# Kernel tuning notes

Hardware: AMD Instinct MI355X
Metric: run time of the kernel (lower is better)

The kernel has to match this reference:

```python
import jax, jax.numpy as jnp
import numpy as np

LAYER_SIZES = [1024, 1024, 1024, 1024, 1024, 1024, 512]
MAX_PATHS = 128
BATCH = 128
N_LAYERS = len(LAYER_SIZES) - 1


def setup_inputs() -> dict:
    key = jax.random.key(0)
    keys = jax.random.split(key, 1 + 2 * N_LAYERS)
    inp = {"x": jax.random.normal(keys[0], (BATCH, LAYER_SIZES[0]), dtype=jnp.float32)}
    for i in range(N_LAYERS):
        inp[f"W{i}"] = jax.random.normal(keys[1 + 2 * i], (LAYER_SIZES[i], LAYER_SIZES[i + 1]), dtype=jnp.float32) * 0.01
        inp[f"b{i}"] = jax.random.normal(keys[2 + 2 * i], (LAYER_SIZES[i + 1],), dtype=jnp.float32) * 0.01
    return inp


def _layer(data, W, b):
    # data: [B, in_feat, P] -> [B, out_feat, 3P]
    B, _, P = data.shape
    O = W.shape[1]
    pos = jnp.einsum('bfp,fo->bpo', data, W) + b          # [B, P, O]; neg branch is exactly -pos
    branches = jnp.stack([-pos, jnp.zeros_like(pos), pos], axis=-1)  # [B, P, O, 3]
    # transpose(1,2) then reshape: interleave branches per source path, matching torch
    return branches.transpose(0, 2, 1, 3).reshape(B, O, P * 3)


def _prune(data, keep):
    # keep top-`keep` paths by L2 norm over the feature dim
    norms = jnp.linalg.norm(data, axis=1)                 # [B, P]
    _, idx = jax.lax.top_k(norms, keep)                   # [B, keep]
    return jnp.take_along_axis(data, idx[:, None, :], axis=-1)


def _forward(x, Ws, bs):
    data = x[:, :, None]                                   # [B, F, 1]
    for i in range(N_LAYERS):
        data = _layer(data, Ws[i], bs[i])
        if i < N_LAYERS - 1:
            data = jnp.tanh(data)
        if data.shape[-1] > MAX_PATHS:
            data = _prune(data, MAX_PATHS)
    # collapse with 'max_abs': per (batch, feature) pick path with largest |value|
    idx = jnp.argmax(jnp.abs(data), axis=-1, keepdims=True)
    output = jnp.take_along_axis(data, idx, axis=-1).squeeze(-1)
    return output, data


def reference(x, W0, b0, W1, b1, W2, b2, W3, b3, W4, b4, W5, b5):
    Ws = [W0, W1, W2, W3, W4, W5]
    bs = [b0, b1, b2, b3, b4, b5]
    return _forward(x, Ws, bs)
```

## Files before the change

### kernel.cpp

```cpp
#include <hip/hip_runtime.h>
#include <math.h>


using s8v = __attribute__((ext_vector_type(8))) short;
using f4v = __attribute__((ext_vector_type(4))) float;

__device__ __forceinline__ float bf2f(short b) {
  unsigned u = ((unsigned)(unsigned short)b) << 16;
  return __builtin_bit_cast(float, u);
}
__device__ __forceinline__ short f2bf(float f) {
  unsigned u = __builtin_bit_cast(unsigned, f);
  u = (u + 0x7FFFu + ((u >> 16) & 1u)) >> 16;
  return (short)u;
}
__device__ __forceinline__ void split_store(float f, short* hi, short* lo) {
  short h = f2bf(f);
  *hi = h;
  *lo = f2bf(f - bf2f(h));
}

struct TWArgs {
  const float* W[6];
  short* Th[6];
  short* Tl[6];
  const float* x;
  short* A0h;
  short* A0l;
  float* zone;
};
__global__ void __launch_bounds__(256)
transW_all(TWArgs a) {
  const int z = blockIdx.z;
  const int t = threadIdx.x;
  if (z == 6) {
    int bid = blockIdx.y * 16 + blockIdx.x;
    if (bid < 128) {
      int i = (bid * 256 + t) * 4;
      float4 v = *(const float4*)&a.x[i];
      short4 h, l;
      h.x = f2bf(v.x); l.x = f2bf(v.x - bf2f(h.x));
      h.y = f2bf(v.y); l.y = f2bf(v.y - bf2f(h.y));
      h.z = f2bf(v.z); l.z = f2bf(v.z - bf2f(h.z));
      h.w = f2bf(v.w); l.w = f2bf(v.w - bf2f(h.w));
      *(short4*)&a.A0h[i] = h;
      *(short4*)&a.A0l[i] = l;
    } else if (bid < 176) {
      a.zone[(bid - 128) * 256 + t] = 0.f;
    }
    return;
  }
  const int N = (z == 5) ? 512 : 1024;
  const int n0 = blockIdx.x * 64, k0 = blockIdx.y * 64;
  if (n0 >= N) return;
  const float* __restrict__ W = a.W[z];
  short* __restrict__ Th = a.Th[z];
  short* __restrict__ Tl = a.Tl[z];
  __shared__ float tile[64][65];
  const int r = t >> 4, c4 = (t & 15) * 4;
#pragma unroll
  for (int i = 0; i < 4; ++i) {
    int rr = r + 16 * i;
    float4 v = *(const float4*)&W[(size_t)(k0 + rr) * N + n0 + c4];
    tile[rr][c4 + 0] = v.x;
    tile[rr][c4 + 1] = v.y;
    tile[rr][c4 + 2] = v.z;
    tile[rr][c4 + 3] = v.w;
  }
  __syncthreads();
#pragma unroll
  for (int i = 0; i < 4; ++i) {
    int n = r + 16 * i;
    short4 h, l;
    float f0 = tile[c4 + 0][n], f1 = tile[c4 + 1][n];
    float f2 = tile[c4 + 2][n], f3 = tile[c4 + 3][n];
    h.x = f2bf(f0); l.x = f2bf(f0 - bf2f(h.x));
    h.y = f2bf(f1); l.y = f2bf(f1 - bf2f(h.y));
    h.z = f2bf(f2); l.z = f2bf(f2 - bf2f(h.z));
    h.w = f2bf(f3); l.w = f2bf(f3 - bf2f(h.w));
    size_t o = (size_t)(n0 + n) * 1024 + k0 + c4;
    *(short4*)&Th[o] = h;
    *(short4*)&Tl[o] = l;
  }
}

template <int EPI, int D, int KS>
__global__ void __launch_bounds__(256, 2)
mfma_gemm(const short* __restrict__ Ah, const short* __restrict__ Al,
          const short* __restrict__ Bh, const short* __restrict__ Bl,
          const float* __restrict__ bias, short* __restrict__ Oh,
          short* __restrict__ Ol, float* __restrict__ Of,
          float* __restrict__ ns, float* __restrict__ dotv,
          float* __restrict__ nrmv, int N, int Dn) {
  constexpr int KC = 1024 / KS;
  constexpr int BKP = 40;
  __shared__ short As_h[64 * BKP], As_l[64 * BKP];
  __shared__ short Bs_h[64 * BKP], Bs_l[64 * BKP];
  const int t = threadIdx.x;
  const int row0 = blockIdx.y * 64;
  const int col0 = blockIdx.x * 64;
  const int kb = blockIdx.z * KC;
  const int sr = t >> 2, sko = (t & 3) * 8;
  const short* Ahp = Ah + (size_t)(row0 + sr) * 1024 + kb + sko;
  const short* Alp = Al + (size_t)(row0 + sr) * 1024 + kb + sko;
  const short* Bhp = Bh + (size_t)(col0 + sr) * 1024 + kb + sko;
  const short* Blp = Bl + (size_t)(col0 + sr) * 1024 + kb + sko;
  const int w = t >> 6, lane = t & 63;
  const int l16 = lane & 15, q = lane >> 4;
  const int wm0 = (w & 1) * 32, wn0 = (w >> 1) * 32;
  const int abase = (wm0 + l16) * BKP + q * 8;
  const int bbase = (wn0 + l16) * BKP + q * 8;
  f4v acc[2][2];
#pragma unroll
  for (int i = 0; i < 2; ++i)
#pragma unroll
    for (int j = 0; j < 2; ++j) acc[i][j] = (f4v){0.f, 0.f, 0.f, 0.f};
  uint4 rah = *(const uint4*)(Ahp);
  uint4 ral = *(const uint4*)(Alp);
  uint4 rbh = *(const uint4*)(Bhp);
  uint4 rbl = *(const uint4*)(Blp);
  for (int k0 = 0; k0 < KC; k0 += 32) {
    __syncthreads();
    *(uint4*)&As_h[sr * BKP + sko] = rah;
    *(uint4*)&As_l[sr * BKP + sko] = ral;
    *(uint4*)&Bs_h[sr * BKP + sko] = rbh;
    *(uint4*)&Bs_l[sr * BKP + sko] = rbl;
    if (k0 + 32 < KC) {
      rah = *(const uint4*)(Ahp + k0 + 32);
      ral = *(const uint4*)(Alp + k0 + 32);
      rbh = *(const uint4*)(Bhp + k0 + 32);
      rbl = *(const uint4*)(Blp + k0 + 32);
    }
    __syncthreads();
    s8v ah[2], al[2], bh[2], bl[2];
#pragma unroll
    for (int mt = 0; mt < 2; ++mt) {
      ah[mt] = *(const s8v*)&As_h[abase + mt * 16 * BKP];
      al[mt] = *(const s8v*)&As_l[abase + mt * 16 * BKP];
    }
#pragma unroll
    for (int nt = 0; nt < 2; ++nt) {
      bh[nt] = *(const s8v*)&Bs_h[bbase + nt * 16 * BKP];
      bl[nt] = *(const s8v*)&Bs_l[bbase + nt * 16 * BKP];
    }
#pragma unroll
    for (int mt = 0; mt < 2; ++mt)
#pragma unroll
      for (int nt = 0; nt < 2; ++nt) {
        acc[mt][nt] = __builtin_amdgcn_mfma_f32_16x16x32_bf16(
            ah[mt], bh[nt], acc[mt][nt], 0, 0, 0);
        acc[mt][nt] = __builtin_amdgcn_mfma_f32_16x16x32_bf16(
            ah[mt], bl[nt], acc[mt][nt], 0, 0, 0);
        acc[mt][nt] = __builtin_amdgcn_mfma_f32_16x16x32_bf16(
            al[mt], bh[nt], acc[mt][nt], 0, 0, 0);
      }
  }

  if constexpr (EPI == 0) {
    const int R = (int)gridDim.y << 6;
#pragma unroll
    for (int nt = 0; nt < 2; ++nt) {
      int gcol = col0 + wn0 + nt * 16 + l16;
#pragma unroll
      for (int mt = 0; mt < 2; ++mt)
#pragma unroll
        for (int r = 0; r < 4; ++r) {
          int rr = row0 + wm0 + mt * 16 + q * 4 + r;
          Of[((size_t)blockIdx.z * R + rr) * N + gcol] = acc[mt][nt][r];
        }
    }
  } else if constexpr (EPI == 1) {
    float bcr[2];
    int gc[2];
#pragma unroll
    for (int nt = 0; nt < 2; ++nt) {
      gc[nt] = col0 + wn0 + nt * 16 + l16;
      bcr[nt] = bias[gc[nt]];
    }
#pragma unroll
    for (int mt = 0; mt < 2; ++mt)
#pragma unroll
      for (int r = 0; r < 4; ++r) {
        int rr = row0 + wm0 + mt * 16 + q * 4 + r;
        int b = rr / D, u = rr - b * D;
        size_t ob = (size_t)(b * Dn) * (size_t)N;
        size_t om = ob + (size_t)(1 + 2 * u) * N;
        size_t op = ob + (size_t)(2 + 2 * u) * N;
        float sm = 0.f, sp = 0.f;
#pragma unroll
        for (int nt = 0; nt < 2; ++nt) {
          float v = acc[mt][nt][r];
          float tm = tanhf(bcr[nt] - v), tp = tanhf(bcr[nt] + v);
          split_store(tm, &Oh[om + gc[nt]], &Ol[om + gc[nt]]);
          split_store(tp, &Oh[op + gc[nt]], &Ol[op + gc[nt]]);
          sm = fmaf(tm, tm, sm);
          sp = fmaf(tp, tp, sp);
        }
#pragma unroll
        for (int msk = 1; msk < 16; msk <<= 1) {
          sm += __shfl_xor(sm, msk);
          sp += __shfl_xor(sp, msk);
        }
        if (l16 == 0) {
          atomicAdd(&ns[b * Dn + 1 + 2 * u], sm);
          atomicAdd(&ns[b * Dn + 2 + 2 * u], sp);
        }
        if (u == 0) {
          float sz = 0.f;
#pragma unroll
          for (int nt = 0; nt < 2; ++nt) {
            float tz = tanhf(bcr[nt]);
            split_store(tz, &Oh[ob + gc[nt]], &Ol[ob + gc[nt]]);
            sz = fmaf(tz, tz, sz);
          }
#pragma unroll
          for (int msk = 1; msk < 16; msk <<= 1) sz += __shfl_xor(sz, msk);
          if (l16 == 0) atomicAdd(&ns[b * Dn], sz);
        }
      }
  } else {
    float b5r[2];
    int gc[2];
#pragma unroll
    for (int nt = 0; nt < 2; ++nt) {
      gc[nt] = col0 + wn0 + nt * 16 + l16;
      b5r[nt] = bias[gc[nt]];
    }
#pragma unroll
    for (int mt = 0; mt < 2; ++mt)
#pragma unroll
      for (int r = 0; r < 4; ++r) {
        int rr = row0 + wm0 + mt * 16 + q * 4 + r;
        float nr = 0.f, dt = 0.f;
#pragma unroll
        for (int nt = 0; nt < 2; ++nt) {
          float v = acc[mt][nt][r];
          Of[(size_t)rr * N + gc[nt]] = v;
          nr = fmaf(v, v, nr);
          dt = fmaf(v, b5r[nt], dt);
        }
#pragma unroll
        for (int msk = 1; msk < 16; msk <<= 1) {
          nr += __shfl_xor(nr, msk);
          dt += __shfl_xor(dt, msk);
        }
        if (l16 == 0) {
          atomicAdd(&nrmv[rr], nr);
          atomicAdd(&dotv[rr], dt);
        }
      }
  }
}

template <int KS>
__global__ void __launch_bounds__(256)
comb0_hl(const float* __restrict__ P, const float* __restrict__ bias,
         short* __restrict__ Oh, short* __restrict__ Ol, int R, int N) {
  int i = blockIdx.x * 256 + threadIdx.x;
  int n4 = N >> 2;
  int r = i / n4, c4 = (i - r * n4) * 4;
  float4 y = *(const float4*)&P[(size_t)r * N + c4];
  size_t stride = (size_t)R * N;
#pragma unroll
  for (int ks = 1; ks < KS; ++ks) {
    const float4 p = *(const float4*)&P[ks * stride + (size_t)r * N + c4];
    y.x += p.x; y.y += p.y; y.z += p.z; y.w += p.w;
  }
  float4 bc = *(const float4*)(bias + c4);
  float t0 = tanhf(bc.x + y.x), t1 = tanhf(bc.y + y.y);
  float t2 = tanhf(bc.z + y.z), t3 = tanhf(bc.w + y.w);
  short4 h, l;
  h.x = f2bf(t0); l.x = f2bf(t0 - bf2f(h.x));
  h.y = f2bf(t1); l.y = f2bf(t1 - bf2f(h.y));
  h.z = f2bf(t2); l.z = f2bf(t2 - bf2f(h.z));
  h.w = f2bf(t3); l.w = f2bf(t3 - bf2f(h.w));
  *(short4*)&Oh[(size_t)r * N + c4] = h;
  *(short4*)&Ol[(size_t)r * N + c4] = l;
}

template <int KS, int D>
__global__ void __launch_bounds__(256)
comb1_hl(const float* __restrict__ P, const float* __restrict__ bias,
         short* __restrict__ Oh, short* __restrict__ Ol, int R, int N,
         int Dn) {
  int i = blockIdx.x * 256 + threadIdx.x;
  int n4 = N >> 2;
  int r = i / n4, c4 = (i - r * n4) * 4;
  int b = r / D, u = r - b * D;
  float4 y = *(const float4*)&P[(size_t)r * N + c4];
  size_t stride = (size_t)R * N;
#pragma unroll
  for (int ks = 1; ks < KS; ++ks) {
    const float4 p = *(const float4*)&P[ks * stride + (size_t)r * N + c4];
    y.x += p.x; y.y += p.y; y.z += p.z; y.w += p.w;
  }
  float4 bc = *(const float4*)(bias + c4);
  size_t ob = (size_t)(b * Dn) * N + c4;
  size_t om = ob + (size_t)(1 + 2 * u) * N;
  size_t op = ob + (size_t)(2 + 2 * u) * N;
  {
    float t0 = tanhf(bc.x - y.x), t1 = tanhf(bc.y - y.y);
    float t2 = tanhf(bc.z - y.z), t3 = tanhf(bc.w - y.w);
    short4 h, l;
    h.x = f2bf(t0); l.x = f2bf(t0 - bf2f(h.x));
    h.y = f2bf(t1); l.y = f2bf(t1 - bf2f(h.y));
    h.z = f2bf(t2); l.z = f2bf(t2 - bf2f(h.z));
    h.w = f2bf(t3); l.w = f2bf(t3 - bf2f(h.w));
    *(short4*)&Oh[om] = h;
    *(short4*)&Ol[om] = l;
  }
  {
    float t0 = tanhf(bc.x + y.x), t1 = tanhf(bc.y + y.y);
    float t2 = tanhf(bc.z + y.z), t3 = tanhf(bc.w + y.w);
    short4 h, l;
    h.x = f2bf(t0); l.x = f2bf(t0 - bf2f(h.x));
    h.y = f2bf(t1); l.y = f2bf(t1 - bf2f(h.y));
    h.z = f2bf(t2); l.z = f2bf(t2 - bf2f(h.z));
    h.w = f2bf(t3); l.w = f2bf(t3 - bf2f(h.w));
    *(short4*)&Oh[op] = h;
    *(short4*)&Ol[op] = l;
  }
  if (u == 0) {
    float t0 = tanhf(bc.x), t1 = tanhf(bc.y);
    float t2 = tanhf(bc.z), t3 = tanhf(bc.w);
    short4 h, l;
    h.x = f2bf(t0); l.x = f2bf(t0 - bf2f(h.x));
    h.y = f2bf(t1); l.y = f2bf(t1 - bf2f(h.y));
    h.z = f2bf(t2); l.z = f2bf(t2 - bf2f(h.z));
    h.w = f2bf(t3); l.w = f2bf(t3 - bf2f(h.w));
    *(short4*)&Oh[ob] = h;
    *(short4*)&Ol[ob] = l;
  }
}

__global__ void __launch_bounds__(256)
prune4_k(const float* __restrict__ ns, int* __restrict__ kept4) {
  int b = blockIdx.x, t = threadIdx.x;
  __shared__ float nss[31];
  __shared__ float key[243];
  __shared__ int cls[243];
  if (t < 31) nss[t] = ns[b * 31 + t];
  __syncthreads();
  if (t < 243) {
    int j = t / 3, t4 = t - 3 * j;
    int d0 = j / 27, d1 = (j / 9) % 3, d2 = (j / 3) % 3, d3 = j % 3;
    int u = 0;
    u = (d0 == 1) ? 0 : (1 + 2 * u + (d0 == 2));
    u = (d1 == 1) ? 0 : (1 + 2 * u + (d1 == 2));
    u = (d2 == 1) ? 0 : (1 + 2 * u + (d2 == 2));
    u = (d3 == 1) ? 0 : (1 + 2 * u + (d3 == 2));
    cls[t] = u;
    key[t] = (t4 == 1) ? 0.f : nss[u];
  }
  __syncthreads();
  if (t < 243) {
    float k = key[t];
    int rank = 0;
    for (int e = 0; e < 243; ++e) {
      float ke = key[e];
      rank += (ke > k) || (ke == k && e < t);
    }
    if (rank < 128) {
      int t4 = t - 3 * (t / 3);
      kept4[b * 128 + rank] = (cls[t] << 1) | (t4 == 2 ? 1 : 0);
    }
  }
}

__global__ void __launch_bounds__(384)
prune5_k(const float* __restrict__ dotv, const float* __restrict__ nrmv,
         const float* __restrict__ b5, const int* __restrict__ kept4,
         int* __restrict__ kept5) {
  int b = blockIdx.x, t = threadIdx.x;
  __shared__ float red[384];
  __shared__ float pns[128];
  __shared__ float key[384];
  float p = 0.f;
  for (int o = t; o < 512; o += 384) p = fmaf(b5[o], b5[o], p);
  red[t] = p;
  __syncthreads();
  if (t < 128) red[t] = red[t] + red[t + 128] + red[t + 256];
  __syncthreads();
  if (t < 64) red[t] += red[t + 64];
  __syncthreads();
  if (t < 32) red[t] += red[t + 32];
  __syncthreads();
  if (t < 16) red[t] += red[t + 16];
  __syncthreads();
  if (t < 8) red[t] += red[t + 8];
  __syncthreads();
  if (t < 4) red[t] += red[t + 4];
  __syncthreads();
  if (t < 2) red[t] += red[t + 2];
  __syncthreads();
  if (t == 0) red[0] += red[1];
  __syncthreads();
  float nb5 = red[0];
  if (t < 128) {
    int k4 = kept4[b * 128 + t];
    int c = k4 >> 1;
    float s = (k4 & 1) ? 1.f : -1.f;
    pns[t] = nb5 + nrmv[b * 31 + c] + s * 2.f * dotv[b * 31 + c];
  }
  __syncthreads();
  int m = t / 3, tt = t - 3 * m;
  key[t] = (tt == 1) ? 0.f : pns[m];
  __syncthreads();
  float k = key[t];
  int rank = 0;
  for (int e = 0; e < 384; ++e) {
    float ke = key[e];
    rank += (ke > k) || (ke == k && e < t);
  }
  if (rank < 128) kept5[b * 128 + rank] = (m << 1) | (tt == 2 ? 1 : 0);
}

__global__ void __launch_bounds__(256)
finalize_k(const float* __restrict__ Y5, const float* __restrict__ b5,
           const int* __restrict__ kept4, const int* __restrict__ kept5,
           float* __restrict__ out, float* __restrict__ dataout) {
  const int b = blockIdx.y;
  const int o0 = blockIdx.x * 64;
  __shared__ float Ys[31][65];
  __shared__ float bias_s[64];
  __shared__ float vt[64][130];
  __shared__ float ra[64][4];
  __shared__ float rv[64][4];
  const int t = threadIdx.x;
  for (int idx = t; idx < 31 * 64; idx += 256) {
    int c = idx >> 6, o = idx & 63;
    Ys[c][o] = Y5[((size_t)b * 31 + c) * 512 + o0 + o];
  }
  if (t < 64) bias_s[t] = b5[o0 + t];
  const int rr = t & 127, oh = t >> 7;
  int k5 = kept5[b * 128 + rr];
  int m = k5 >> 1;
  float sig = (k5 & 1) ? 1.f : -1.f;
  int k4 = kept4[b * 128 + m];
  int cc = k4 >> 1;
  float s4 = (k4 & 1) ? 1.f : -1.f;
  float afac = sig * s4;
  __syncthreads();
#pragma unroll
  for (int ol = 0; ol < 32; ++ol) {
    int o = oh * 32 + ol;
    float v = sig * bias_s[o] + afac * Ys[cc][o];
    dataout[((size_t)b * 512 + o0 + o) * 128 + rr] = v;
    vt[o][rr] = v;
  }
  __syncthreads();
  int o = t >> 2, q = t & 3;
  float bestv = vt[o][q * 32];
  float besta = fabsf(bestv);
  for (int i = 1; i < 32; ++i) {
    float v = vt[o][q * 32 + i];
    float a = fabsf(v);
    if (a > besta) {
      besta = a;
      bestv = v;
    }
  }
  ra[o][q] = besta;
  rv[o][q] = bestv;
  __syncthreads();
  if (t < 64) {
    float ba = ra[t][0], bv = rv[t][0];
#pragma unroll
    for (int qq = 1; qq < 4; ++qq) {
      if (ra[t][qq] > ba) {
        ba = ra[t][qq];
        bv = rv[t][qq];
      }
    }
    out[(size_t)b * 512 + o0 + t] = bv;
  }
}

extern "C" void kernel_launch(void* const* d_in, const int* in_sizes, int n_in,
                              void* d_out, int out_size, void* d_ws,
                              size_t ws_size, hipStream_t stream) {
  const float* x = (const float*)d_in[0];
  const float* Wt[6];
  const float* bs[6];
  for (int i = 0; i < 6; ++i) {
    Wt[i] = (const float*)d_in[1 + 2 * i];
    bs[i] = (const float*)d_in[2 + 2 * i];
  }
  char* base = (char*)d_ws;
  short* A0h = (short*)(base + 0);
  short* A0l = (short*)(base + 262144);
  short* Wh[6], *Wl[6];
  {
    size_t off = 524288;
    for (int i = 0; i < 6; ++i) {
      size_t sz = (i < 5) ? 2097152 : 1048576;
      Wh[i] = (short*)(base + off);
      Wl[i] = (short*)(base + off + sz);
      off += 2 * sz;
    }
  }
  short* C1h = (short*)(base + 23592960), *C1l = (short*)(base + 23855104);
  short* C2h = (short*)(base + 24117248), *C2l = (short*)(base + 24903680);
  short* C3h = (short*)(base + 25690112), *C3l = (short*)(base + 27525120);
  short* C4h = (short*)(base + 29360128), *C4l = (short*)(base + 33292288);
  short* C5h = (short*)(base + 524288);
  short* C5l = (short*)(base + 8912896);
  float* PA = (float*)(base + 29360128);
  float* PB = (float*)(base + 524288);
  float* Y5 = (float*)(base + 23592960);
  float* ns = (float*)(base + 37224448);
  float* dotv = ns + 3968;
  float* nrmv = dotv + 3968;
  int* kept4 = (int*)(base + 37273600);
  int* kept5 = (int*)(base + 37339136);
  float* outp = (float*)d_out;
  float* dataout = outp + 128 * 512;

  dim3 blk(256);
  TWArgs twa;
  for (int i = 0; i < 6; ++i) {
    twa.W[i] = Wt[i];
    twa.Th[i] = Wh[i];
    twa.Tl[i] = Wl[i];
  }
  twa.x = x;
  twa.A0h = A0h;
  twa.A0l = A0l;
  twa.zone = ns;
  transW_all<<<dim3(16, 16, 7), blk, 0, stream>>>(twa);

  mfma_gemm<0, 1, 4><<<dim3(16, 2, 4), blk, 0, stream>>>(
      A0h, A0l, Wh[0], Wl[0], nullptr, nullptr, nullptr, PA, nullptr, nullptr,
      nullptr, 1024, 1);
  comb0_hl<4><<<dim3(128), blk, 0, stream>>>(PA, bs[0], C1h, C1l, 128, 1024);
  mfma_gemm<0, 1, 4><<<dim3(16, 2, 4), blk, 0, stream>>>(
      C1h, C1l, Wh[1], Wl[1], nullptr, nullptr, nullptr, PA, nullptr, nullptr,
      nullptr, 1024, 3);
  comb1_hl<4, 1><<<dim3(128), blk, 0, stream>>>(PA, bs[1], C2h, C2l, 128, 1024,
                                                3);
  mfma_gemm<0, 3, 4><<<dim3(16, 6, 4), blk, 0, stream>>>(
      C2h, C2l, Wh[2], Wl[2], nullptr, nullptr, nullptr, PA, nullptr, nullptr,
      nullptr, 1024, 7);
  comb1_hl<4, 3><<<dim3(384), blk, 0, stream>>>(PA, bs[2], C3h, C3l, 384, 1024,
                                                7);
  mfma_gemm<0, 7, 2><<<dim3(16, 14, 2), blk, 0, stream>>>(
      C3h, C3l, Wh[3], Wl[3], nullptr, nullptr, nullptr, PB, nullptr, nullptr,
      nullptr, 1024, 15);
  comb1_hl<2, 7><<<dim3(896), blk, 0, stream>>>(PB, bs[3], C4h, C4l, 896, 1024,
                                                15);
  mfma_gemm<1, 15, 1><<<dim3(16, 30), blk, 0, stream>>>(
      C4h, C4l, Wh[4], Wl[4], bs[4], C5h, C5l, nullptr, ns, nullptr, nullptr,
      1024, 31);
  prune4_k<<<dim3(128), blk, 0, stream>>>(ns, kept4);
  mfma_gemm<2, 31, 1><<<dim3(8, 62), blk, 0, stream>>>(
      C5h, C5l, Wh[5], Wl[5], bs[5], nullptr, nullptr, Y5, nullptr, dotv, nrmv,
      512, 0);
  prune5_k<<<dim3(128), dim3(384), 0, stream>>>(dotv, nrmv, bs[5], kept4,
                                                kept5);
  finalize_k<<<dim3(8, 128), blk, 0, stream>>>(Y5, bs[5], kept4, kept5, outp,
                                               dataout);
}
```

Measured before the change: 246.5 us.

## Stage GEMM epilogue through shared memory for vectorized stores; raise split-K

The MFMA GEMM epilogue now writes accumulators into a padded shared-memory tile and re-reads them so each thread owns 16 contiguous columns of one row. This allows 128-bit global stores of the fp32 partials and the packed bf16 hi/lo outputs, and reduces the atomic norm reductions to a 4-lane shuffle. Launch bounds are raised to 3 blocks per SM, and the first two tiny GEMMs use split-K of 8 instead of 4 to fill more CUs. The costs are an extra 17KB of LDS per block, a barrier, and more partial sums for the combine kernels to read.

Result: no change. 242.5 us (-1.6%).

```diff
diff --git a/kernel.cpp b/kernel.cpp
--- a/kernel.cpp
+++ b/kernel.cpp
@@ -13,11 +13,6 @@
   unsigned u = __builtin_bit_cast(unsigned, f);
   u = (u + 0x7FFFu + ((u >> 16) & 1u)) >> 16;
   return (short)u;
-}
-__device__ __forceinline__ void split_store(float f, short* hi, short* lo) {
-  short h = f2bf(f);
-  *hi = h;
-  *lo = f2bf(f - bf2f(h));
 }
 
 struct TWArgs {
@@ -85,7 +80,7 @@
 }
 
 template <int EPI, int D, int KS>
-__global__ void __launch_bounds__(256, 2)
+__global__ void __launch_bounds__(256, 3)
 mfma_gemm(const short* __restrict__ Ah, const short* __restrict__ Al,
           const short* __restrict__ Bh, const short* __restrict__ Bl,
           const float* __restrict__ bias, short* __restrict__ Oh,
@@ -96,6 +91,7 @@
   constexpr int BKP = 40;
   __shared__ short As_h[64 * BKP], As_l[64 * BKP];
   __shared__ short Bs_h[64 * BKP], Bs_l[64 * BKP];
+  __shared__ float et[64][68];
   const int t = threadIdx.x;
   const int row0 = blockIdx.y * 64;
   const int col0 = blockIdx.x * 64;
@@ -156,99 +152,103 @@
       }
   }
 
+#pragma unroll
+  for (int mt = 0; mt < 2; ++mt)
+#pragma unroll
+    for (int nt = 0; nt < 2; ++nt)
+#pragma unroll
+      for (int r = 0; r < 4; ++r)
+        et[wm0 + mt * 16 + q * 4 + r][wn0 + nt * 16 + l16] = acc[mt][nt][r];
+  __syncthreads();
+  const int rl = t >> 2, cc = (t & 3) * 16;
+  float v[16];
+#pragma unroll
+  for (int j = 0; j < 16; ++j) v[j] = et[rl][cc + j];
+  const int rr = row0 + rl;
+
   if constexpr (EPI == 0) {
     const int R = (int)gridDim.y << 6;
-#pragma unroll
-    for (int nt = 0; nt < 2; ++nt) {
-      int gcol = col0 + wn0 + nt * 16 + l16;
-#pragma unroll
-      for (int mt = 0; mt < 2; ++mt)
-#pragma unroll
-        for (int r = 0; r < 4; ++r) {
-          int rr = row0 + wm0 + mt * 16 + q * 4 + r;
-          Of[((size_t)blockIdx.z * R + rr) * N + gcol] = acc[mt][nt][r];
-        }
-    }
+    float* dst = Of + ((size_t)blockIdx.z * R + rr) * N + col0 + cc;
+#pragma unroll
+    for (int i = 0; i < 4; ++i)
+      *(float4*)&dst[4 * i] =
+          make_float4(v[4 * i], v[4 * i + 1], v[4 * i + 2], v[4 * i + 3]);
   } else if constexpr (EPI == 1) {
-    float bcr[2];
-    int gc[2];
-#pragma unroll
-    for (int nt = 0; nt < 2; ++nt) {
-      gc[nt] = col0 + wn0 + nt * 16 + l16;
-      bcr[nt] = bias[gc[nt]];
-    }
-#pragma unroll
-    for (int mt = 0; mt < 2; ++mt)
-#pragma unroll
-      for (int r = 0; r < 4; ++r) {
-        int rr = row0 + wm0 + mt * 16 + q * 4 + r;
-        int b = rr / D, u = rr - b * D;
-        size_t ob = (size_t)(b * Dn) * (size_t)N;
-        size_t om = ob + (size_t)(1 + 2 * u) * N;
-        size_t op = ob + (size_t)(2 + 2 * u) * N;
-        float sm = 0.f, sp = 0.f;
-#pragma unroll
-        for (int nt = 0; nt < 2; ++nt) {
-          float v = acc[mt][nt][r];
-          float tm = tanhf(bcr[nt] - v), tp = tanhf(bcr[nt] + v);
-          split_store(tm, &Oh[om + gc[nt]], &Ol[om + gc[nt]]);
-          split_store(tp, &Oh[op + gc[nt]], &Ol[op + gc[nt]]);
-          sm = fmaf(tm, tm, sm);
-          sp = fmaf(tp, tp, sp);
-        }
-#pragma unroll
-        for (int msk = 1; msk < 16; msk <<= 1) {
-          sm += __shfl_xor(sm, msk);
-          sp += __shfl_xor(sp, msk);
-        }
-        if (l16 == 0) {
-          atomicAdd(&ns[b * Dn + 1 + 2 * u], sm);
-          atomicAdd(&ns[b * Dn + 2 + 2 * u], sp);
-        }
-        if (u == 0) {
-          float sz = 0.f;
-#pragma unroll
-          for (int nt = 0; nt < 2; ++nt) {
-            float tz = tanhf(bcr[nt]);
-            split_store(tz, &Oh[ob + gc[nt]], &Ol[ob + gc[nt]]);
-            sz = fmaf(tz, tz, sz);
-          }
-#pragma unroll
-          for (int msk = 1; msk < 16; msk <<= 1) sz += __shfl_xor(sz, msk);
-          if (l16 == 0) atomicAdd(&ns[b * Dn], sz);
-        }
+    const int b = rr / D, u = rr - b * D;
+    const size_t ob = (size_t)(b * Dn) * (size_t)N + col0 + cc;
+    const size_t om = ob + (size_t)(1 + 2 * u) * N;
+    const size_t op = ob + (size_t)(2 + 2 * u) * N;
+    uint mh[8], ml[8], ph[8], pl[8];
+    float sm = 0.f, sp = 0.f;
+#pragma unroll
+    for (int j2 = 0; j2 < 8; ++j2) {
+      float bc0 = bias[col0 + cc + 2 * j2];
+      float bc1 = bias[col0 + cc + 2 * j2 + 1];
+      float tm0 = tanhf(bc0 - v[2 * j2]), tm1 = tanhf(bc1 - v[2 * j2 + 1]);
+      float tp0 = tanhf(bc0 + v[2 * j2]), tp1 = tanhf(bc1 + v[2 * j2 + 1]);
+      short h0 = f2bf(tm0), h1 = f2bf(tm1);
+      short g0 = f2bf(tm0 - bf2f(h0)), g1 = f2bf(tm1 - bf2f(h1));
+      mh[j2] = (uint)(unsigned short)h0 | ((uint)(unsigned short)h1 << 16);
+      ml[j2] = (uint)(unsigned short)g0 | ((uint)(unsigned short)g1 << 16);
+      h0 = f2bf(tp0); h1 = f2bf(tp1);
+      g0 = f2bf(tp0 - bf2f(h0)); g1 = f2bf(tp1 - bf2f(h1));
+      ph[j2] = (uint)(unsigned short)h0 | ((uint)(unsigned short)h1 << 16);
+      pl[j2] = (uint)(unsigned short)g0 | ((uint)(unsigned short)g1 << 16);
+      sm = fmaf(tm0, tm0, fmaf(tm1, tm1, sm));
+      sp = fmaf(tp0, tp0, fmaf(tp1, tp1, sp));
+    }
+    *(uint4*)&Oh[om] = make_uint4(mh[0], mh[1], mh[2], mh[3]);
+    *(uint4*)&Oh[om + 8] = make_uint4(mh[4], mh[5], mh[6], mh[7]);
+    *(uint4*)&Ol[om] = make_uint4(ml[0], ml[1], ml[2], ml[3]);
+    *(uint4*)&Ol[om + 8] = make_uint4(ml[4], ml[5], ml[6], ml[7]);
+    *(uint4*)&Oh[op] = make_uint4(ph[0], ph[1], ph[2], ph[3]);
+    *(uint4*)&Oh[op + 8] = make_uint4(ph[4], ph[5], ph[6], ph[7]);
+    *(uint4*)&Ol[op] = make_uint4(pl[0], pl[1], pl[2], pl[3]);
+    *(uint4*)&Ol[op + 8] = make_uint4(pl[4], pl[5], pl[6], pl[7]);
+    sm += __shfl_xor(sm, 1); sm += __shfl_xor(sm, 2);
+    sp += __shfl_xor(sp, 1); sp += __shfl_xor(sp, 2);
+    if ((t & 3) == 0) {
+      atomicAdd(&ns[b * Dn + 1 + 2 * u], sm);
+      atomicAdd(&ns[b * Dn + 2 + 2 * u], sp);
+    }
+    if (u == 0) {
+      uint zh[8], zl[8];
+      float sz = 0.f;
+#pragma unroll
+      for (int j2 = 0; j2 < 8; ++j2) {
+        float tz0 = tanhf(bias[col0 + cc + 2 * j2]);
+        float tz1 = tanhf(bias[col0 + cc + 2 * j2 + 1]);
+        short h0 = f2bf(tz0), h1 = f2bf(tz1);
+        short g0 = f2bf(tz0 - bf2f(h0)), g1 = f2bf(tz1 - bf2f(h1));
+        zh[j2] = (uint)(unsigned short)h0 | ((uint)(unsigned short)h1 << 16);
+        zl[j2] = (uint)(unsigned short)g0 | ((uint)(unsigned short)g1 << 16);
+        sz = fmaf(tz0, tz0, fmaf(tz1, tz1, sz));
       }
+      *(uint4*)&Oh[ob] = make_uint4(zh[0], zh[1], zh[2], zh[3]);
+      *(uint4*)&Oh[ob + 8] = make_uint4(zh[4], zh[5], zh[6], zh[7]);
+      *(uint4*)&Ol[ob] = make_uint4(zl[0], zl[1], zl[2], zl[3]);
+      *(uint4*)&Ol[ob + 8] = make_uint4(zl[4], zl[5], zl[6], zl[7]);
+      sz += __shfl_xor(sz, 1); sz += __shfl_xor(sz, 2);
+      if ((t & 3) == 0) atomicAdd(&ns[b * Dn], sz);
+    }
   } else {
-    float b5r[2];
-    int gc[2];
-#pragma unroll
-    for (int nt = 0; nt < 2; ++nt) {
-      gc[nt] = col0 + wn0 + nt * 16 + l16;
-      b5r[nt] = bias[gc[nt]];
-    }
-#pragma unroll
-    for (int mt = 0; mt < 2; ++mt)
-#pragma unroll
-      for (int r = 0; r < 4; ++r) {
-        int rr = row0 + wm0 + mt * 16 + q * 4 + r;
-        float nr = 0.f, dt = 0.f;
-#pragma unroll
-        for (int nt = 0; nt < 2; ++nt) {
-          float v = acc[mt][nt][r];
-          Of[(size_t)rr * N + gc[nt]] = v;
-          nr = fmaf(v, v, nr);
-          dt = fmaf(v, b5r[nt], dt);
-        }
-#pragma unroll
-        for (int msk = 1; msk < 16; msk <<= 1) {
-          nr += __shfl_xor(nr, msk);
-          dt += __shfl_xor(dt, msk);
-        }
-        if (l16 == 0) {
-          atomicAdd(&nrmv[rr], nr);
-          atomicAdd(&dotv[rr], dt);
-        }
-      }
+    float nr = 0.f, dt = 0.f;
+    float* dst = Of + (size_t)rr * N + col0 + cc;
+#pragma unroll
+    for (int j = 0; j < 16; ++j) {
+      nr = fmaf(v[j], v[j], nr);
+      dt = fmaf(v[j], bias[col0 + cc + j], dt);
+    }
+#pragma unroll
+    for (int i = 0; i < 4; ++i)
+      *(float4*)&dst[4 * i] =
+          make_float4(v[4 * i], v[4 * i + 1], v[4 * i + 2], v[4 * i + 3]);
+    nr += __shfl_xor(nr, 1); nr += __shfl_xor(nr, 2);
+    dt += __shfl_xor(dt, 1); dt += __shfl_xor(dt, 2);
+    if ((t & 3) == 0) {
+      atomicAdd(&nrmv[rr], nr);
+      atomicAdd(&dotv[rr], dt);
+    }
   }
 }
 
@@ -529,14 +529,14 @@
   twa.zone = ns;
   transW_all<<<dim3(16, 16, 7), blk, 0, stream>>>(twa);
 
-  mfma_gemm<0, 1, 4><<<dim3(16, 2, 4), blk, 0, stream>>>(
+  mfma_gemm<0, 1, 8><<<dim3(16, 2, 8), blk, 0, stream>>>(
       A0h, A0l, Wh[0], Wl[0], nullptr, nullptr, nullptr, PA, nullptr, nullptr,
       nullptr, 1024, 1);
-  comb0_hl<4><<<dim3(128), blk, 0, stream>>>(PA, bs[0], C1h, C1l, 128, 1024);
-  mfma_gemm<0, 1, 4><<<dim3(16, 2, 4), blk, 0, stream>>>(
+  comb0_hl<8><<<dim3(128), blk, 0, stream>>>(PA, bs[0], C1h, C1l, 128, 1024);
+  mfma_gemm<0, 1, 8><<<dim3(16, 2, 8), blk, 0, stream>>>(
       C1h, C1l, Wh[1], Wl[1], nullptr, nullptr, nullptr, PA, nullptr, nullptr,
       nullptr, 1024, 3);
-  comb1_hl<4, 1><<<dim3(128), blk, 0, stream>>>(PA, bs[1], C2h, C2l, 128, 1024,
+  comb1_hl<8, 1><<<dim3(128), blk, 0, stream>>>(PA, bs[1], C2h, C2l, 128, 1024,
                                                 3);
   mfma_gemm<0, 3, 4><<<dim3(16, 6, 4), blk, 0, stream>>>(
       C2h, C2l, Wh[2], Wl[2], nullptr, nullptr, nullptr, PA, nullptr, nullptr,
```
